# Kernel optimization log

Hardware: AMD Instinct MI355X
Metric: run time of the kernel (lower is better)

## Reference

```python
import jax, jax.numpy as jnp
import numpy as np

M, IN, OUT, R = 8192, 4096, 4096, 16  # tokens, in_features, out_features, lora rank


def setup_inputs() -> dict:
    key = jax.random.key(0)
    k = jax.random.split(key, 7)
    # symmetric int8 quantized activations and weights
    x = jax.random.randint(k[0], (M, IN), -127, 128, dtype=jnp.int8)
    weight = jax.random.randint(k[1], (OUT, IN), -127, 128, dtype=jnp.int8)
    # per-token activation scales and per-output-channel weight scales
    x_scales = jax.random.uniform(k[2], (M,), jnp.float32, 0.5, 1.5) / 127.0
    scales = jax.random.uniform(k[3], (OUT,), jnp.float32, 0.5, 1.5) / 127.0
    bias = jax.random.normal(k[4], (OUT,), jnp.float32)
    # module inits lora_a ~ N(0, 1/r); lora_b is zeros in the module but we use
    # small random values so the LoRA path is numerically exercised
    lora_a = jax.random.normal(k[5], (R, IN), jnp.float32) * (1.0 / R)
    lora_b = jax.random.normal(k[6], (OUT, R), jnp.float32) * 0.02
    return dict(x=x, weight=weight, bias=bias, x_scales=x_scales,
                scales=scales, lora_a=lora_a, lora_b=lora_b, fuse_gelu=1)


def reference(x, weight, bias, x_scales, scales, lora_a, lora_b, fuse_gelu):
    acc = jax.lax.dot_general(x, weight, (((1,), (1,)), ((), ())),
                              preferred_element_type=jnp.int32)
    # dequantize with outer product of per-token and per-channel scales
    main = acc.astype(jnp.float32) * x_scales[:, None] * scales[None, :]
    # LoRA correction on the dequantized activations: (x_deq @ A^T) @ B^T
    x_deq = x.astype(jnp.float32) * x_scales[:, None]          # [M, IN]
    lora = (x_deq @ lora_a.T) @ lora_b.T                        # [M, R] @ [R, OUT]
    out = main + lora + bias[None, :]
    if fuse_gelu:  # static Python flag
        out = jax.nn.gelu(out, approximate=True)  # tanh-approx GELU (CUDA fused path)
    return out
```

## Files before the change

kernel.cpp:

```cpp
#include <hip/hip_runtime.h>

#define M_DIM 8192
#define IN_DIM 4096
#define OUT_DIM 4096

typedef int   v4i  __attribute__((ext_vector_type(4)));
typedef int   v16i __attribute__((ext_vector_type(16)));
typedef short v8s  __attribute__((ext_vector_type(8)));
typedef float v4f  __attribute__((ext_vector_type(4)));
typedef float v16f __attribute__((ext_vector_type(16)));

static __device__ __forceinline__ int pack4(int a, int b, int c, int d) {
    return (a & 255) | ((b & 255) << 8) | ((c & 255) << 16) | ((d & 255) << 24);
}

static __device__ __forceinline__ short f2bf(float f) {
    unsigned u = __float_as_uint(f);
    u = (u + 0x7FFFu + ((u >> 16) & 1u)) >> 16;
    return (short)u;
}

static __device__ __forceinline__ short i2bf(int v) {
    float f = (float)v;
    return (short)(__float_as_uint(f) >> 16);
}

static __device__ __forceinline__ float gelu_tanh(float u) {
    float u2 = u * u;
    float p  = fmaf(u2, 0.0356774081f, 0.7978845608f);
    float v  = u * p;
    float e  = __builtin_amdgcn_exp2f(v * 2.8853900818f);
    return u - u * __builtin_amdgcn_rcpf(e + 1.0f);
}

static __device__ __forceinline__ void async_cp16(const signed char* g, signed char* l) {
    __builtin_amdgcn_global_load_lds((const __attribute__((address_space(1))) void*)g,
                                     (__attribute__((address_space(3))) void*)l, 16, 0, 0);
}


__global__ __launch_bounds__(256) void pack_a_kernel(const float* __restrict__ la,
                                                     short* __restrict__ a16) {
    size_t i = ((size_t)blockIdx.x * 256 + threadIdx.x) * 8;
    const float4* p = (const float4*)(la + i);
    float4 a = p[0], b = p[1];
    v8s o;
    o[0] = f2bf(a.x); o[1] = f2bf(a.y); o[2] = f2bf(a.z); o[3] = f2bf(a.w);
    o[4] = f2bf(b.x); o[5] = f2bf(b.y); o[6] = f2bf(b.z); o[7] = f2bf(b.w);
    *(v8s*)(a16 + i) = o;
}

__global__ __launch_bounds__(256) void pack_w_kernel(const int* __restrict__ w,
                                                     signed char* __restrict__ w8t) {
    const int flat = blockIdx.x * 256 + threadIdx.x;
    const int l  = flat & 63;
    const int gp = (flat >> 6) & 15;
    const int kk = (flat >> 10) & 63;
    const int bn = flat >> 16;
    const int n = bn * 256 + ((gp >> 1) << 5) + (l & 31);
    const int k = kk * 64 + ((gp & 1) << 5) + ((l >> 5) << 4);
    const int4* p = (const int4*)(w + (size_t)n * IN_DIM + k);
    int4 a = p[0], b = p[1], c = p[2], d = p[3];
    int4 o;
    o.x = pack4(a.x, a.y, a.z, a.w);
    o.y = pack4(b.x, b.y, b.z, b.w);
    o.z = pack4(c.x, c.y, c.z, c.w);
    o.w = pack4(d.x, d.y, d.z, d.w);
    *(int4*)(w8t + (size_t)flat * 16) = o;
}

__global__ __launch_bounds__(256) void pack_x_lora_kernel(const int* __restrict__ x,
                                                          const short* __restrict__ a16,
                                                          signed char* __restrict__ x8t,
                                                          float* __restrict__ T) {
    __shared__ float red[4 * 256];
    const int tid = threadIdx.x;
    const int lane = tid & 63, wv = tid >> 6;
    const int fr = lane & 15, fq = lane >> 4;
    const int m0 = blockIdx.x * 16;
    const int bm = m0 >> 8;
    const int g  = (m0 >> 5) & 7;
    const int l5 = (m0 & 16) + fr;
    const int row = m0 + fr;

    v4f acc = {0.f, 0.f, 0.f, 0.f};
#pragma unroll 2
    for (int kt = 0; kt < 32; ++kt) {
        const int k  = wv * 1024 + kt * 32 + fq * 8;
        const int4* xp = (const int4*)(x + (size_t)row * IN_DIM + k);
        int4 a = xp[0], b = xp[1];
        const int kk = k >> 6, c = (k >> 4) & 3, j8 = (k >> 3) & 1;
        int2 pk = make_int2(pack4(a.x, a.y, a.z, a.w), pack4(b.x, b.y, b.z, b.w));
        *(int2*)(x8t + ((size_t)((bm * 64 + kk) * 16 + g * 2 + (c >> 1))) * 1024 +
                 ((c & 1) * 32 + l5) * 16 + j8 * 8) = pk;
        v8s xa;
        xa[0] = i2bf(a.x); xa[1] = i2bf(a.y); xa[2] = i2bf(a.z); xa[3] = i2bf(a.w);
        xa[4] = i2bf(b.x); xa[5] = i2bf(b.y); xa[6] = i2bf(b.z); xa[7] = i2bf(b.w);
        v8s aa = *(const v8s*)(a16 + (size_t)fr * IN_DIM + k);
        acc = __builtin_amdgcn_mfma_f32_16x16x32_bf16(xa, aa, acc, 0, 0, 0);
    }
    *(v4f*)&red[wv * 256 + lane * 4] = acc;
    __syncthreads();

    float s = red[tid] + red[256 + tid] + red[512 + tid] + red[768 + tid];
    const int sl = tid >> 2, j = tid & 3;
    const int r16 = ((sl >> 4) << 2) + j, col = sl & 15;
    T[(size_t)(m0 + r16) * 16 + col] = s;
}

__global__ __launch_bounds__(256, 1) void q8_gemm_kernel(
    const signed char* __restrict__ x8t, const signed char* __restrict__ w8t,
    const float* __restrict__ Tp, const float* __restrict__ lbm,
    const float* __restrict__ bias, const float* __restrict__ xsc,
    const float* __restrict__ wsc, const int* __restrict__ gflag,
    float* __restrict__ out) {
    __shared__ __align__(16) signed char smem[65536];

    const int tid  = threadIdx.x;
    const int lane = tid & 63;
    const int wv   = tid >> 6;
    const int wm   = wv >> 1, wn = wv & 1;
    const int b   = blockIdx.x;
    const int xcd = b & 7, rr = b >> 3;
    const int bm  = xcd * 4 + (rr & 3);
    const int bn  = rr >> 2;

    const int lofs = lane * 16;
    const signed char* Asrc = x8t + (size_t)bm * (64 * 16 * 1024);
    const signed char* Bsrc = w8t + (size_t)bn * (64 * 16 * 1024);
    signed char* ldsA = smem + wv * 4096;
    signed char* ldsB = smem + 16384 + wv * 4096;

    v16i acc[4][4];
    {
        v16i z;
#pragma unroll
        for (int i = 0; i < 16; ++i) z[i] = 0;
#pragma unroll
        for (int mt = 0; mt < 4; ++mt)
#pragma unroll
            for (int nt = 0; nt < 4; ++nt) acc[mt][nt] = z;
    }

    {
        const signed char* as = Asrc + (size_t)(wv * 4) * 1024 + lofs;
        const signed char* bs = Bsrc + (size_t)(wv * 4) * 1024 + lofs;
#pragma unroll
        for (int i = 0; i < 4; ++i) {
            async_cp16(as + i * 1024, ldsA + i * 1024);
            async_cp16(bs + i * 1024, ldsB + i * 1024);
        }
    }

    for (int kk = 0; kk < 64; ++kk) {
        __syncthreads();
        if (kk + 1 < 64) {
            const int nb = (kk + 1) & 1;
            const signed char* as = Asrc + ((size_t)(kk + 1) * 16 + wv * 4) * 1024 + lofs;
            const signed char* bs = Bsrc + ((size_t)(kk + 1) * 16 + wv * 4) * 1024 + lofs;
#pragma unroll
            for (int i = 0; i < 4; ++i) {
                async_cp16(as + i * 1024, ldsA + nb * 32768 + i * 1024);
                async_cp16(bs + i * 1024, ldsB + nb * 32768 + i * 1024);
            }
        }
        const signed char* Ab = smem + (kk & 1) * 32768;
        const signed char* Bb = Ab + 16384;
#pragma unroll
        for (int s = 0; s < 2; ++s) {
            v4i av[4], bv[4];
#pragma unroll
            for (int mt = 0; mt < 4; ++mt)
                av[mt] = *(const v4i*)(Ab + ((wm * 4 + mt) * 2 + s) * 1024 + lofs);
#pragma unroll
            for (int nt = 0; nt < 4; ++nt)
                bv[nt] = *(const v4i*)(Bb + ((wn * 4 + nt) * 2 + s) * 1024 + lofs);
#pragma unroll
            for (int mt = 0; mt < 4; ++mt)
#pragma unroll
                for (int nt = 0; nt < 4; ++nt)
                    acc[mt][nt] = __builtin_amdgcn_mfma_i32_32x32x32_i8(
                        av[mt], bv[nt], acc[mt][nt], 0, 0, 0);
        }
    }

    const int mbase = bm * 256 + wm * 128;
    const int nbase = bn * 256 + wn * 128;
    const int l31 = lane & 31, lh = lane >> 5;
    const bool dg = (*gflag) != 0;

    v8s tf[4], bf[4];
#pragma unroll
    for (int mt = 0; mt < 4; ++mt) {
        const float* t0 = Tp + (size_t)(mbase + mt * 32 + l31) * 16 + lh * 8;
        v8s v;
#pragma unroll
        for (int j = 0; j < 8; ++j) v[j] = f2bf(t0[j]);
        tf[mt] = v;
    }
#pragma unroll
    for (int nt = 0; nt < 4; ++nt) {
        const float* bp = lbm + (size_t)(nbase + nt * 32 + l31) * 16 + lh * 8;
        v8s v;
#pragma unroll
        for (int j = 0; j < 8; ++j) v[j] = f2bf(bp[j]);
        bf[nt] = v;
    }
    float wsa[4], bba[4];
#pragma unroll
    for (int nt = 0; nt < 4; ++nt) {
        const int col = nbase + nt * 32 + l31;
        wsa[nt] = wsc[col];
        bba[nt] = bias[col];
    }

#pragma unroll
    for (int mt = 0; mt < 4; ++mt) {
        const int rowb = mbase + mt * 32 + lh * 4;
        float4 xs0 = *(const float4*)(xsc + rowb);
        float4 xs1 = *(const float4*)(xsc + rowb + 8);
        float4 xs2 = *(const float4*)(xsc + rowb + 16);
        float4 xs3 = *(const float4*)(xsc + rowb + 24);
        float xsv[16] = {xs0.x, xs0.y, xs0.z, xs0.w, xs1.x, xs1.y, xs1.z, xs1.w,
                         xs2.x, xs2.y, xs2.z, xs2.w, xs3.x, xs3.y, xs3.z, xs3.w};
#pragma unroll
        for (int nt = 0; nt < 4; ++nt) {
            v16f fa;
#pragma unroll
            for (int i = 0; i < 16; ++i) fa[i] = (float)acc[mt][nt][i] * wsa[nt];
            fa = __builtin_amdgcn_mfma_f32_32x32x16_bf16(tf[mt], bf[nt], fa, 0, 0, 0);
            const int col = nbase + nt * 32 + l31;
#pragma unroll
            for (int r = 0; r < 16; ++r) {
                float u = fmaf(xsv[r], fa[r], bba[nt]);
                if (dg) u = gelu_tanh(u);
                out[(size_t)(rowb + (r & 3) + 8 * (r >> 2)) * OUT_DIM + col] = u;
            }
        }
    }
}

extern "C" void kernel_launch(void* const* d_in, const int* in_sizes, int n_in,
                              void* d_out, int out_size, void* d_ws, size_t ws_size,
                              hipStream_t stream) {
    const int*   x     = (const int*)d_in[0];
    const int*   wt    = (const int*)d_in[1];
    const float* bias  = (const float*)d_in[2];
    const float* xsc   = (const float*)d_in[3];
    const float* wsc   = (const float*)d_in[4];
    const float* la    = (const float*)d_in[5];
    const float* lb    = (const float*)d_in[6];
    const int*   gflag = (const int*)d_in[7];
    float* out = (float*)d_out;

    signed char* x8t = (signed char*)d_ws;
    signed char* w8t = x8t + (size_t)M_DIM * IN_DIM;
    float* T = (float*)(w8t + (size_t)OUT_DIM * IN_DIM);
    short* a16 = (short*)w8t;

    pack_a_kernel<<<16 * IN_DIM / (8 * 256), 256, 0, stream>>>(la, a16);
    pack_x_lora_kernel<<<M_DIM / 16, 256, 0, stream>>>(x, a16, x8t, T);
    pack_w_kernel<<<(size_t)OUT_DIM * IN_DIM / (16 * 256), 256, 0, stream>>>(wt, w8t);
    q8_gemm_kernel<<<(M_DIM / 256) * (OUT_DIM / 256), 256, 0, stream>>>(
        x8t, w8t, T, lb, bias, xsc, wsc, gflag, out);
}
```

Measured before the change: 445.5 us.

## Restructure int8 GEMM main loop into 8-wave, triple-buffered, ping-pong schedule

Moves the GEMM from 4 waves to 8 waves per block, each computing a 128x64 subtile, and replaces the double-buffered loop with a three-stage LDS ring. Global-to-LDS async copies are interleaved with MFMA clusters, separated by s_barrier and s_setprio so loads and matrix math overlap. The aim is to hide memory latency and keep the matrix units busy. It adds more barriers, needs 96KB of LDS, and relies on hand-placed vmcnt waits that are fragile; launch_bounds(512,2) with 96KB LDS may not actually fit two blocks per CU.

Result: no change. 436.8 us (-1.9%).

```diff
diff --git a/kernel.cpp b/kernel.cpp
--- a/kernel.cpp
+++ b/kernel.cpp
@@ -108,30 +108,29 @@
     T[(size_t)(m0 + r16) * 16 + col] = s;
 }
 
-__global__ __launch_bounds__(256, 1) void q8_gemm_kernel(
+__global__ __launch_bounds__(512, 2) void q8_gemm_kernel(
     const signed char* __restrict__ x8t, const signed char* __restrict__ w8t,
     const float* __restrict__ Tp, const float* __restrict__ lbm,
     const float* __restrict__ bias, const float* __restrict__ xsc,
     const float* __restrict__ wsc, const int* __restrict__ gflag,
     float* __restrict__ out) {
-    __shared__ __align__(16) signed char smem[65536];
+    __shared__ __align__(16) signed char smem[98304];
 
     const int tid  = threadIdx.x;
     const int lane = tid & 63;
     const int wv   = tid >> 6;
-    const int wm   = wv >> 1, wn = wv & 1;
+    const int wm   = wv >> 2, wn = wv & 3;
     const int b   = blockIdx.x;
     const int xcd = b & 7, rr = b >> 3;
     const int bm  = xcd * 4 + (rr & 3);
     const int bn  = rr >> 2;
 
     const int lofs = lane * 16;
+    const size_t toff = (size_t)tid * 16;
     const signed char* Asrc = x8t + (size_t)bm * (64 * 16 * 1024);
     const signed char* Bsrc = w8t + (size_t)bn * (64 * 16 * 1024);
-    signed char* ldsA = smem + wv * 4096;
-    signed char* ldsB = smem + 16384 + wv * 4096;
-
-    v16i acc[4][4];
+
+    v16i acc[4][2];
     {
         v16i z;
 #pragma unroll
@@ -139,57 +138,99 @@
 #pragma unroll
         for (int mt = 0; mt < 4; ++mt)
 #pragma unroll
-            for (int nt = 0; nt < 4; ++nt) acc[mt][nt] = z;
-    }
-
-    {
-        const signed char* as = Asrc + (size_t)(wv * 4) * 1024 + lofs;
-        const signed char* bs = Bsrc + (size_t)(wv * 4) * 1024 + lofs;
-#pragma unroll
-        for (int i = 0; i < 4; ++i) {
-            async_cp16(as + i * 1024, ldsA + i * 1024);
-            async_cp16(bs + i * 1024, ldsB + i * 1024);
+            for (int nt = 0; nt < 2; ++nt) acc[mt][nt] = z;
+    }
+
+#pragma unroll
+    for (int tt = 0; tt < 2; ++tt) {
+        const signed char* ga = Asrc + (size_t)tt * 16384 + toff;
+        const signed char* gb = Bsrc + (size_t)tt * 16384 + toff;
+        signed char* l = smem + tt * 32768 + (wv << 10);
+        async_cp16(ga,        l);
+        async_cp16(ga + 8192, l + 8192);
+        async_cp16(gb,        l + 16384);
+        async_cp16(gb + 8192, l + 24576);
+    }
+    asm volatile("s_waitcnt vmcnt(4)" ::: "memory");
+    __builtin_amdgcn_s_barrier();
+
+    int cur = 0;
+    for (int t = 0; t < 64; ++t) {
+        const signed char* Ab = smem + cur * 32768;
+        const signed char* Bb = Ab + 16384;
+        const int sb = (cur == 0) ? 2 : cur - 1;
+        signed char* sl = smem + sb * 32768 + (wv << 10);
+        const signed char* ga = Asrc + (size_t)(t + 2) * 16384 + toff;
+        const signed char* gb = Bsrc + (size_t)(t + 2) * 16384 + toff;
+        const bool pf = (t < 62);
+
+        v4i a0, a1, a2, a3, b0, b1;
+
+        a0 = *(const v4i*)(Ab + (wm * 8 + 0) * 1024 + lofs);
+        a1 = *(const v4i*)(Ab + (wm * 8 + 2) * 1024 + lofs);
+        b0 = *(const v4i*)(Bb + (wn * 4 + 0) * 1024 + lofs);
+        b1 = *(const v4i*)(Bb + (wn * 4 + 2) * 1024 + lofs);
+        if (pf) async_cp16(ga, sl);
+        __builtin_amdgcn_s_barrier();
+        __builtin_amdgcn_s_setprio(1);
+        acc[0][0] = __builtin_amdgcn_mfma_i32_32x32x32_i8(a0, b0, acc[0][0], 0, 0, 0);
+        acc[0][1] = __builtin_amdgcn_mfma_i32_32x32x32_i8(a0, b1, acc[0][1], 0, 0, 0);
+        acc[1][0] = __builtin_amdgcn_mfma_i32_32x32x32_i8(a1, b0, acc[1][0], 0, 0, 0);
+        acc[1][1] = __builtin_amdgcn_mfma_i32_32x32x32_i8(a1, b1, acc[1][1], 0, 0, 0);
+        __builtin_amdgcn_s_setprio(0);
+        __builtin_amdgcn_s_barrier();
+
+        a2 = *(const v4i*)(Ab + (wm * 8 + 4) * 1024 + lofs);
+        a3 = *(const v4i*)(Ab + (wm * 8 + 6) * 1024 + lofs);
+        if (pf) async_cp16(ga + 8192, sl + 8192);
+        __builtin_amdgcn_s_barrier();
+        __builtin_amdgcn_s_setprio(1);
+        acc[2][0] = __builtin_amdgcn_mfma_i32_32x32x32_i8(a2, b0, acc[2][0], 0, 0, 0);
+        acc[2][1] = __builtin_amdgcn_mfma_i32_32x32x32_i8(a2, b1, acc[2][1], 0, 0, 0);
+        acc[3][0] = __builtin_amdgcn_mfma_i32_32x32x32_i8(a3, b0, acc[3][0], 0, 0, 0);
+        acc[3][1] = __builtin_amdgcn_mfma_i32_32x32x32_i8(a3, b1, acc[3][1], 0, 0, 0);
+        __builtin_amdgcn_s_setprio(0);
+        __builtin_amdgcn_s_barrier();
+
+        a0 = *(const v4i*)(Ab + (wm * 8 + 1) * 1024 + lofs);
+        a1 = *(const v4i*)(Ab + (wm * 8 + 3) * 1024 + lofs);
+        b0 = *(const v4i*)(Bb + (wn * 4 + 1) * 1024 + lofs);
+        b1 = *(const v4i*)(Bb + (wn * 4 + 3) * 1024 + lofs);
+        if (pf) async_cp16(gb, sl + 16384);
+        __builtin_amdgcn_s_barrier();
+        __builtin_amdgcn_s_setprio(1);
+        acc[0][0] = __builtin_amdgcn_mfma_i32_32x32x32_i8(a0, b0, acc[0][0], 0, 0, 0);
+        acc[0][1] = __builtin_amdgcn_mfma_i32_32x32x32_i8(a0, b1, acc[0][1], 0, 0, 0);
+        acc[1][0] = __builtin_amdgcn_mfma_i32_32x32x32_i8(a1, b0, acc[1][0], 0, 0, 0);
+        acc[1][1] = __builtin_amdgcn_mfma_i32_32x32x32_i8(a1, b1, acc[1][1], 0, 0, 0);
+        __builtin_amdgcn_s_setprio(0);
+        __builtin_amdgcn_s_barrier();
+
+        a2 = *(const v4i*)(Ab + (wm * 8 + 5) * 1024 + lofs);
+        a3 = *(const v4i*)(Ab + (wm * 8 + 7) * 1024 + lofs);
+        if (pf) async_cp16(gb + 8192, sl + 24576);
+        __builtin_amdgcn_s_barrier();
+        __builtin_amdgcn_s_setprio(1);
+        acc[2][0] = __builtin_amdgcn_mfma_i32_32x32x32_i8(a2, b0, acc[2][0], 0, 0, 0);
+        acc[2][1] = __builtin_amdgcn_mfma_i32_32x32x32_i8(a2, b1, acc[2][1], 0, 0, 0);
+        acc[3][0] = __builtin_amdgcn_mfma_i32_32x32x32_i8(a3, b0, acc[3][0], 0, 0, 0);
+        acc[3][1] = __builtin_amdgcn_mfma_i32_32x32x32_i8(a3, b1, acc[3][1], 0, 0, 0);
+        __builtin_amdgcn_s_setprio(0);
+        if (pf) {
+            asm volatile("s_waitcnt vmcnt(4)" ::: "memory");
+        } else if (t == 62) {
+            asm volatile("s_waitcnt vmcnt(0)" ::: "memory");
         }
-    }
-
-    for (int kk = 0; kk < 64; ++kk) {
-        __syncthreads();
-        if (kk + 1 < 64) {
-            const int nb = (kk + 1) & 1;
-            const signed char* as = Asrc + ((size_t)(kk + 1) * 16 + wv * 4) * 1024 + lofs;
-            const signed char* bs = Bsrc + ((size_t)(kk + 1) * 16 + wv * 4) * 1024 + lofs;
-#pragma unroll
-            for (int i = 0; i < 4; ++i) {
-                async_cp16(as + i * 1024, ldsA + nb * 32768 + i * 1024);
-                async_cp16(bs + i * 1024, ldsB + nb * 32768 + i * 1024);
-            }
-        }
-        const signed char* Ab = smem + (kk & 1) * 32768;
-        const signed char* Bb = Ab + 16384;
-#pragma unroll
-        for (int s = 0; s < 2; ++s) {
-            v4i av[4], bv[4];
-#pragma unroll
-            for (int mt = 0; mt < 4; ++mt)
-                av[mt] = *(const v4i*)(Ab + ((wm * 4 + mt) * 2 + s) * 1024 + lofs);
-#pragma unroll
-            for (int nt = 0; nt < 4; ++nt)
-                bv[nt] = *(const v4i*)(Bb + ((wn * 4 + nt) * 2 + s) * 1024 + lofs);
-#pragma unroll
-            for (int mt = 0; mt < 4; ++mt)
-#pragma unroll
-                for (int nt = 0; nt < 4; ++nt)
-                    acc[mt][nt] = __builtin_amdgcn_mfma_i32_32x32x32_i8(
-                        av[mt], bv[nt], acc[mt][nt], 0, 0, 0);
-        }
+        __builtin_amdgcn_s_barrier();
+        cur = (cur == 2) ? 0 : cur + 1;
     }
 
     const int mbase = bm * 256 + wm * 128;
-    const int nbase = bn * 256 + wn * 128;
+    const int nbase = bn * 256 + wn * 64;
     const int l31 = lane & 31, lh = lane >> 5;
     const bool dg = (*gflag) != 0;
 
-    v8s tf[4], bf[4];
+    v8s tf[4], bf[2];
 #pragma unroll
     for (int mt = 0; mt < 4; ++mt) {
         const float* t0 = Tp + (size_t)(mbase + mt * 32 + l31) * 16 + lh * 8;
@@ -199,16 +240,16 @@
         tf[mt] = v;
     }
 #pragma unroll
-    for (int nt = 0; nt < 4; ++nt) {
+    for (int nt = 0; nt < 2; ++nt) {
         const float* bp = lbm + (size_t)(nbase + nt * 32 + l31) * 16 + lh * 8;
         v8s v;
 #pragma unroll
         for (int j = 0; j < 8; ++j) v[j] = f2bf(bp[j]);
         bf[nt] = v;
     }
-    float wsa[4], bba[4];
-#pragma unroll
-    for (int nt = 0; nt < 4; ++nt) {
+    float wsa[2], bba[2];
+#pragma unroll
+    for (int nt = 0; nt < 2; ++nt) {
         const int col = nbase + nt * 32 + l31;
         wsa[nt] = wsc[col];
         bba[nt] = bias[col];
@@ -224,7 +265,7 @@
         float xsv[16] = {xs0.x, xs0.y, xs0.z, xs0.w, xs1.x, xs1.y, xs1.z, xs1.w,
                          xs2.x, xs2.y, xs2.z, xs2.w, xs3.x, xs3.y, xs3.z, xs3.w};
 #pragma unroll
-        for (int nt = 0; nt < 4; ++nt) {
+        for (int nt = 0; nt < 2; ++nt) {
             v16f fa;
 #pragma unroll
             for (int i = 0; i < 16; ++i) fa[i] = (float)acc[mt][nt][i] * wsa[nt];
@@ -261,6 +302,6 @@
     pack_a_kernel<<<16 * IN_DIM / (8 * 256), 256, 0, stream>>>(la, a16);
     pack_x_lora_kernel<<<M_DIM / 16, 256, 0, stream>>>(x, a16, x8t, T);
     pack_w_kernel<<<(size_t)OUT_DIM * IN_DIM / (16 * 256), 256, 0, stream>>>(wt, w8t);
-    q8_gemm_kernel<<<(M_DIM / 256) * (OUT_DIM / 256), 256, 0, stream>>>(
+    q8_gemm_kernel<<<(M_DIM / 256) * (OUT_DIM / 256), 512, 0, stream>>>(
         x8t, w8t, T, lb, bias, xsc, wsc, gflag, out);
 }
```
